# Kernel tuning notes

Measured on AMD Instinct MI355X. Metric: run time of the kernel, lower is better.

Reference implementation:

```python
import jax, jax.numpy as jnp
import numpy as np

N = 1024       # nodes
D1 = 64        # hidden_dim_1
D2 = 64        # hidden_dim_2
E = 16384      # edges
P = 8192       # query pairs
MAXX = 100     # max node label -> Embedding(MAXX+1, D1)
EPS = 1e-5     # LayerNorm eps (no affine)


def _ln(t):
    m = jnp.mean(t, axis=-1, keepdims=True)
    v = jnp.mean((t - m) ** 2, axis=-1, keepdims=True)
    return (t - m) / jnp.sqrt(v + EPS)


def setup_inputs() -> dict:
    key = jax.random.key(0)
    ks = jax.random.split(key, 12)
    s = 0.1
    x = jax.random.randint(ks[0], (N,), 0, MAXX + 1)
    ei = jax.random.randint(ks[1], (2, E), 0, N)
    pos = jax.random.randint(ks[2], (P, 2), 0, N)
    emb = jax.random.normal(ks[3], (MAXX + 1, D1)) * s
    sage_Wl = jax.random.normal(ks[4], (2, D1, D1)) * s   # lin_l weight (aggr path, has bias)
    sage_bl = jnp.zeros((2, D1))
    sage_Wr = jax.random.normal(ks[5], (2, D1, D1)) * s   # lin_r weight (root path, no bias)
    h_W = jax.random.normal(ks[6], (D1 + 1, D2)) * s
    h_b = jnp.zeros((D2,))
    g_W = jax.random.normal(ks[7], (D1 + 1 + 2 * D2, D2)) * s
    g_b = jnp.zeros((D2,))
    lin_W = jax.random.normal(ks[8], (D2, 1)) * s
    lin_b = jnp.zeros((1,))
    return {"x": x, "ei": ei, "pos": pos, "emb": emb,
            "sage_Wl": sage_Wl, "sage_bl": sage_bl, "sage_Wr": sage_Wr,
            "h_W": h_W, "h_b": h_b, "g_W": g_W, "g_b": g_b,
            "lin_W": lin_W, "lin_b": lin_b}


def reference(x, ei, pos, emb, sage_Wl, sage_bl, sage_Wr, h_W, h_b, g_W, g_b, lin_W, lin_b):
    n = N
    src, dst = ei[0], ei[1]
    h = emb[x]                                            # (n, D1)
    # SAGEConv x2: mean-aggregate src->dst, lin_l(aggr)+bias + lin_r(root); then LN (no affine, no relu)
    deg = jax.ops.segment_sum(jnp.ones((E,), h.dtype), dst, num_segments=n)
    deg = jnp.maximum(deg, 1.0)[:, None]
    for i in range(2):
        aggr = jax.ops.segment_sum(h[src], dst, num_segments=n) / deg
        h = _ln(aggr @ sage_Wl[i] + sage_bl[i] + h @ sage_Wr[i])
    # pairwise outer product features: (n, n, D1)
    A = h[:, None, :] * h[None, :, :]
    eim = jnp.zeros((n * n,), h.dtype).at[src * n + dst].set(1.0).reshape(n, n, 1)
    A = jnp.concatenate([A, eim], axis=-1)                # (n, n, D1+1)
    # mataggr: B = h_1(A); row/col sums; D = cat(A, vec_p, vec_q); g_1(D)
    B = jax.nn.relu(_ln(A @ h_W + h_b))                   # (n, n, D2)
    vec_p = jnp.sum(B, axis=1, keepdims=True)             # (n, 1, D2)
    vec_q = jnp.sum(B, axis=0, keepdims=True)             # (1, n, D2)
    Dm = jnp.concatenate([A,
                          jnp.broadcast_to(vec_p, (n, n, D2)),
                          jnp.broadcast_to(vec_q, (n, n, D2))], axis=-1)
    G = jax.nn.relu(_ln(Dm @ g_W + g_b))                  # (n, n, D2)
    # symmetrize and gather query pairs
    S = (G * jnp.transpose(G, (1, 0, 2))).reshape(n * n, D2)
    sel = S[pos[:, 0] * n + pos[:, 1]]                    # (P, D2)
    return sel @ lin_W + lin_b                            # (P, 1)
```

## Files before the change

### kernel.cpp

```cpp
#include <hip/hip_runtime.h>
#include <hip/hip_bf16.h>

#define NN 1024
#define DD 64
#define EE 16384
#define PP 8192
#define EPSF 1e-5f
#define SWP (DD + 8)

typedef __hip_bfloat16 bf16;
typedef __attribute__((ext_vector_type(8))) short short8;
typedef __attribute__((ext_vector_type(4))) float f32x4;

static __device__ __forceinline__ float dec1(const void* src, int i, int fl) {
    if (fl) return ((const float*)src)[i];
    return __bfloat162float(((const bf16*)src)[i]);
}
static __device__ __forceinline__ unsigned short f2bf_u(float f) {
    bf16 h = __float2bfloat16(f);
    return *reinterpret_cast<unsigned short*>(&h);
}
static __device__ __forceinline__ float bfu2f(unsigned short u) {
    unsigned int b = ((unsigned int)u) << 16;
    return __uint_as_float(b);
}

__global__ void k_probe(const unsigned short* __restrict__ raw, int n, int* __restrict__ flag) {
    int i = blockIdx.x * blockDim.x + threadIdx.x;
    if (i >= n) return;
    unsigned int bits = ((unsigned int)raw[i]) << 16;
    float v = __uint_as_float(bits);
    if (!(fabsf(v) <= 1e3f)) atomicOr(flag, 1);
}

__global__ void k_prep(const void* __restrict__ emb, const void* __restrict__ sWl,
                       const void* __restrict__ sbl, const void* __restrict__ sWr,
                       const void* __restrict__ hW, const void* __restrict__ hb,
                       const void* __restrict__ gW, const void* __restrict__ gb,
                       const void* __restrict__ lW, const void* __restrict__ lb,
                       const int* __restrict__ x, const int* __restrict__ ei,
                       const int* __restrict__ flagp,
                       float* __restrict__ Wlf, float* __restrict__ blf, float* __restrict__ Wrf,
                       float* __restrict__ WfT, float* __restrict__ hbw,
                       float* __restrict__ gWf, float* __restrict__ linf,
                       float* __restrict__ h0, int* __restrict__ deg,
                       unsigned int* __restrict__ eim, unsigned int* __restrict__ eimT) {
    int fl = *flagp;
    int b = blockIdx.x, t = threadIdx.x;
    if (b < 32) {
        int i = b * 256 + t; Wlf[i] = dec1(sWl, i, fl);
    } else if (b < 33) {
        if (t < 128) blf[t] = dec1(sbl, t, fl);
    } else if (b < 65) {
        int i = (b - 33) * 256 + t; Wrf[i] = dec1(sWr, i, fl);
    } else if (b < 82) {
        int i = (b - 65) * 256 + t;
        if (i < 4096) { int n = i >> 6, k = i & 63; WfT[n * DD + k] = dec1(hW, k * DD + n, fl); }
        else if (i < 4160) { hbw[i - 4096] = dec1(hb, i - 4096, fl); }
        else if (i < 4224) { hbw[64 + (i - 4160)] = dec1(hW, 64 * DD + (i - 4160), fl); }
    } else if (b < 131) {
        int i = (b - 82) * 256 + t;
        if (i < 193 * DD) gWf[i] = dec1(gW, i, fl);
        else if (i < 194 * DD) gWf[i] = dec1(gb, i - 193 * DD, fl);
    } else if (b < 132) {
        if (t < DD) linf[t] = dec1(lW, t, fl);
        else if (t == DD) linf[DD] = dec1(lb, 0, fl);
    } else if (b < 388) {
        int i = (b - 132) * 256 + t;
        int node = i >> 6, f = i & 63;
        h0[i] = dec1(emb, x[node] * DD + f, fl);
    } else {
        int e = (b - 388) * 256 + t;
        if (e < EE) {
            int s = ei[e], d = ei[EE + e];
            atomicAdd(&deg[d], 1);
            unsigned int idx = (unsigned int)(s * NN + d);
            atomicOr(&eim[idx >> 5], 1u << (idx & 31));
            unsigned int idxT = (unsigned int)(d * NN + s);
            atomicOr(&eimT[idxT >> 5], 1u << (idxT & 31));
        }
    }
}

__global__ void k_scan(const int* __restrict__ deg, int* __restrict__ rowptr,
                       int* __restrict__ cursor) {
    __shared__ int tmp[NN];
    int t = threadIdx.x;
    int v = deg[t];
    tmp[t] = v;
    __syncthreads();
    for (int off = 1; off < NN; off <<= 1) {
        int add = (t >= off) ? tmp[t - off] : 0;
        __syncthreads();
        tmp[t] += add;
        __syncthreads();
    }
    int incl = tmp[t];
    rowptr[t] = incl - v;
    cursor[t] = incl - v;
    if (t == NN - 1) rowptr[NN] = incl;
}

__global__ void k_scatter(const int* __restrict__ ei, int* __restrict__ cursor,
                          int* __restrict__ csrc) {
    int e = blockIdx.x * blockDim.x + threadIdx.x;
    if (e >= EE) return;
    int d = ei[EE + e];
    int c = atomicAdd(&cursor[d], 1);
    csrc[c] = ei[e];
}

__global__ void k_sage(const int* __restrict__ rowptr, const int* __restrict__ csrc,
                       const float* __restrict__ hin,
                       const float* __restrict__ Wl, const float* __restrict__ bl,
                       const float* __restrict__ Wr,
                       float* __restrict__ hout, unsigned short* __restrict__ hbf) {
    int i = blockIdx.x;
    int f = threadIdx.x;
    __shared__ float sa[DD], sh[DD];
    int r0 = rowptr[i], r1 = rowptr[i + 1];
    float s = 0.f;
    for (int r = r0; r < r1; ++r) {
        int src = csrc[r];
        s += hin[src * DD + f];
    }
    float dg = (float)max(r1 - r0, 1);
    sa[f] = s / dg;
    sh[f] = hin[i * DD + f];
    __syncthreads();
    float o = bl[f];
    for (int k = 0; k < DD; ++k) {
        o += sa[k] * Wl[k * DD + f] + sh[k] * Wr[k * DD + f];
    }
    float m = o;
    for (int off = 32; off; off >>= 1) m += __shfl_xor(m, off);
    m *= (1.0f / DD);
    float d0 = o - m;
    float v = d0 * d0;
    for (int off = 32; off; off >>= 1) v += __shfl_xor(v, off);
    v *= (1.0f / DD);
    float r = d0 * rsqrtf(v + EPSF);
    hout[i * DD + f] = r;
    hbf[i * DD + f] = f2bf_u(r);
}

__launch_bounds__(256)
__global__ void k_bstage(const float* __restrict__ h2, const unsigned short* __restrict__ hbf,
                         const float* __restrict__ WfT, const float* __restrict__ hbw,
                         const unsigned int* __restrict__ eim,
                         const unsigned int* __restrict__ eimT,
                         float* __restrict__ vp_part, float* __restrict__ vq_part) {
    int bid = blockIdx.x;
    int fix = bid >> 1, half = bid & 1;
    int tid = threadIdx.x;
    int lane = tid & 63, wave = tid >> 6;
    int l15 = lane & 15, quad = lane >> 4;

    __shared__ unsigned short sW[DD * SWP];
    __shared__ float red[4][2 * DD];

    {
        int m = tid >> 2;
        int k0 = (tid & 3) * 16;
        const float* hi = h2 + fix * DD;
        const float* wr = WfT + m * DD;
#pragma unroll
        for (int u = 0; u < 16; ++u) {
            int k = k0 + u;
            sW[m * SWP + k] = f2bf_u(hi[k] * wr[k]);
        }
    }
    __syncthreads();

    short8 Af[4][2];
#pragma unroll
    for (int mt = 0; mt < 4; ++mt)
#pragma unroll
        for (int kt = 0; kt < 2; ++kt)
            Af[mt][kt] = *(const short8*)(sW + (mt * 16 + l15) * SWP + kt * 32 + quad * 8);

    float hb0[4][4], hww[4][4];
#pragma unroll
    for (int mt = 0; mt < 4; ++mt) {
        f32x4 a = *(const f32x4*)(hbw + mt * 16 + quad * 4);
        f32x4 wv = *(const f32x4*)(hbw + 64 + mt * 16 + quad * 4);
#pragma unroll
        for (int r = 0; r < 4; ++r) { hb0[mt][r] = a[r]; hww[mt][r] = wv[r]; }
    }

    float accf[4][4], accb[4][4];
#pragma unroll
    for (int mt = 0; mt < 4; ++mt)
#pragma unroll
        for (int r = 0; r < 4; ++r) { accf[mt][r] = 0.f; accb[mt][r] = 0.f; }

    for (int g = half * 32 + wave; g < half * 32 + 32; g += 4) {
        short8 B0 = *(const short8*)(hbf + (g * 16 + l15) * DD + quad * 8);
        short8 B1 = *(const short8*)(hbf + (g * 16 + l15) * DD + 32 + quad * 8);

        f32x4 C[4];
#pragma unroll
        for (int mt = 0; mt < 4; ++mt) C[mt] = (f32x4){0.f, 0.f, 0.f, 0.f};
#pragma unroll
        for (int mt = 0; mt < 4; ++mt)
            C[mt] = __builtin_amdgcn_mfma_f32_16x16x32_bf16(Af[mt][0], B0, C[mt], 0, 0, 0);
#pragma unroll
        for (int mt = 0; mt < 4; ++mt)
            C[mt] = __builtin_amdgcn_mfma_f32_16x16x32_bf16(Af[mt][1], B1, C[mt], 0, 0, 0);

        unsigned int base = (unsigned int)(fix * NN + g * 16);
        unsigned int sf = (eim[base >> 5] >> (base & 31)) & 0xFFFFu;
        unsigned int sb = (eimT[base >> 5] >> (base & 31)) & 0xFFFFu;
        float ef = (float)((sf >> l15) & 1u);

        float s1 = 0.f, s2 = 0.f;
#pragma unroll
        for (int mt = 0; mt < 4; ++mt)
#pragma unroll
            for (int r = 0; r < 4; ++r) {
                float v = C[mt][r] + hb0[mt][r] + ef * hww[mt][r];
                C[mt][r] = v;
                s1 += v;
                s2 += v * v;
            }
        s1 += __shfl_xor(s1, 16); s1 += __shfl_xor(s1, 32);
        s2 += __shfl_xor(s2, 16); s2 += __shfl_xor(s2, 32);
        float mean = s1 * (1.f / DD);
        float var = fmaxf(s2 * (1.f / DD) - mean * mean, 0.f);
        float rs = rsqrtf(var + EPSF);
        float mrs = mean * rs;

        if (sf == sb) {
#pragma unroll
            for (int mt = 0; mt < 4; ++mt)
#pragma unroll
                for (int r = 0; r < 4; ++r) {
                    float u = fmaxf(C[mt][r] * rs - mrs, 0.f);
                    accf[mt][r] += u;
                    accb[mt][r] += u;
                }
        } else {
#pragma unroll
            for (int mt = 0; mt < 4; ++mt)
#pragma unroll
                for (int r = 0; r < 4; ++r)
                    accf[mt][r] += fmaxf(C[mt][r] * rs - mrs, 0.f);
            float de = (float)((sb >> l15) & 1u) - ef;
            float t1 = 0.f, t2 = 0.f;
#pragma unroll
            for (int mt = 0; mt < 4; ++mt)
#pragma unroll
                for (int r = 0; r < 4; ++r) {
                    float v = C[mt][r] + de * hww[mt][r];
                    C[mt][r] = v;
                    t1 += v;
                    t2 += v * v;
                }
            t1 += __shfl_xor(t1, 16); t1 += __shfl_xor(t1, 32);
            t2 += __shfl_xor(t2, 16); t2 += __shfl_xor(t2, 32);
            float mean2 = t1 * (1.f / DD);
            float var2 = fmaxf(t2 * (1.f / DD) - mean2 * mean2, 0.f);
            float rs2 = rsqrtf(var2 + EPSF);
            float mrs2 = mean2 * rs2;
#pragma unroll
            for (int mt = 0; mt < 4; ++mt)
#pragma unroll
                for (int r = 0; r < 4; ++r)
                    accb[mt][r] += fmaxf(C[mt][r] * rs2 - mrs2, 0.f);
        }
    }

#pragma unroll
    for (int step = 1; step < 16; step <<= 1)
#pragma unroll
        for (int mt = 0; mt < 4; ++mt)
#pragma unroll
            for (int r = 0; r < 4; ++r) {
                accf[mt][r] += __shfl_xor(accf[mt][r], step);
                accb[mt][r] += __shfl_xor(accb[mt][r], step);
            }

    if (l15 == 0) {
#pragma unroll
        for (int mt = 0; mt < 4; ++mt)
#pragma unroll
            for (int r = 0; r < 4; ++r) {
                int m = mt * 16 + quad * 4 + r;
                red[wave][m] = accf[mt][r];
                red[wave][DD + m] = accb[mt][r];
            }
    }
    __syncthreads();
    if (tid < 2 * DD) {
        float sum = red[0][tid] + red[1][tid] + red[2][tid] + red[3][tid];
        if (tid < DD) vp_part[(half * NN + fix) * DD + tid] = sum;
        else          vq_part[(half * NN + fix) * DD + (tid - DD)] = sum;
    }
}

__global__ void k_ppqq2(const float* __restrict__ vpp, const float* __restrict__ vqp,
                        const float* __restrict__ gWf,
                        float* __restrict__ ppb, float* __restrict__ qqb) {
    int b = blockIdx.x;
    int f = threadIdx.x;
    int i = b & 1023, which = b >> 10;
    const float* part = which ? vqp : vpp;
    int row0 = which ? 129 : 65;
    __shared__ float sv[DD];
    sv[f] = part[i * DD + f] + part[(NN + i) * DD + f];
    __syncthreads();
    float o = 0.f;
    for (int k = 0; k < DD; ++k) o += sv[k] * gWf[(row0 + k) * DD + f];
    (which ? qqb : ppb)[i * DD + f] = o;
}

__launch_bounds__(256)
__global__ void k_final(const int* __restrict__ pos, const unsigned short* __restrict__ hbf,
                        const float* __restrict__ gWf, const unsigned int* __restrict__ eim,
                        const float* __restrict__ pp, const float* __restrict__ qq,
                        const float* __restrict__ linf, const int* __restrict__ flag,
                        void* __restrict__ outv) {
    int blk = blockIdx.x;
    int tid = threadIdx.x;
    int lane = tid & 63, wave = tid >> 6;
    int l15 = lane & 15, quad = lane >> 4;

    __shared__ unsigned short sgW[DD * SWP];
    __shared__ unsigned short sq[64 * SWP];

    {
        int m = tid >> 2;
        int k0 = (tid & 3) * 16;
#pragma unroll
        for (int u = 0; u < 16; ++u) {
            int k = k0 + u;
            sgW[m * SWP + k] = f2bf_u(gWf[k * DD + m]);
        }
    }
    for (int u = 0; u < 16; ++u) {
        int row = wave * 16 + u;
        int p = blk * 64 + row;
        int a = pos[2 * p], b = pos[2 * p + 1];
        float prod = bfu2f(hbf[a * DD + lane]) * bfu2f(hbf[b * DD + lane]);
        sq[row * SWP + lane] = f2bf_u(prod);
    }
    __syncthreads();

    short8 B0 = *(const short8*)(sq + (wave * 16 + l15) * SWP + quad * 8);
    short8 B1 = *(const short8*)(sq + (wave * 16 + l15) * SWP + 32 + quad * 8);

    f32x4 C[4];
#pragma unroll
    for (int mt = 0; mt < 4; ++mt) C[mt] = (f32x4){0.f, 0.f, 0.f, 0.f};
#pragma unroll
    for (int mt = 0; mt < 4; ++mt) {
        short8 A0 = *(const short8*)(sgW + (mt * 16 + l15) * SWP + quad * 8);
        C[mt] = __builtin_amdgcn_mfma_f32_16x16x32_bf16(A0, B0, C[mt], 0, 0, 0);
    }
#pragma unroll
    for (int mt = 0; mt < 4; ++mt) {
        short8 A1 = *(const short8*)(sgW + (mt * 16 + l15) * SWP + 32 + quad * 8);
        C[mt] = __builtin_amdgcn_mfma_f32_16x16x32_bf16(A1, B1, C[mt], 0, 0, 0);
    }

    int p = blk * 64 + wave * 16 + l15;
    int a = pos[2 * p], b = pos[2 * p + 1];
    unsigned int iab = (unsigned int)(a * NN + b), iba = (unsigned int)(b * NN + a);
    float eab = (float)((eim[iab >> 5] >> (iab & 31)) & 1u);
    float eba = (float)((eim[iba >> 5] >> (iba & 31)) & 1u);

    float u1[4][4], u2[4][4];
    float s1 = 0.f, s12 = 0.f, s2 = 0.f, s22 = 0.f;
#pragma unroll
    for (int mt = 0; mt < 4; ++mt) {
        int m0 = mt * 16 + quad * 4;
        f32x4 w64v = *(const f32x4*)(gWf + 64 * DD + m0);
        f32x4 gbv  = *(const f32x4*)(gWf + 193 * DD + m0);
        f32x4 ppa  = *(const f32x4*)(pp + a * DD + m0);
        f32x4 qqb_ = *(const f32x4*)(qq + b * DD + m0);
        f32x4 ppb_ = *(const f32x4*)(pp + b * DD + m0);
        f32x4 qqa  = *(const f32x4*)(qq + a * DD + m0);
#pragma unroll
        for (int r = 0; r < 4; ++r) {
            float v1 = C[mt][r] + eab * w64v[r] + ppa[r] + qqb_[r] + gbv[r];
            float v2 = C[mt][r] + eba * w64v[r] + ppb_[r] + qqa[r] + gbv[r];
            u1[mt][r] = v1; u2[mt][r] = v2;
            s1 += v1; s12 += v1 * v1;
            s2 += v2; s22 += v2 * v2;
        }
    }
    s1 += __shfl_xor(s1, 16);  s1 += __shfl_xor(s1, 32);
    s12 += __shfl_xor(s12, 16); s12 += __shfl_xor(s12, 32);
    s2 += __shfl_xor(s2, 16);  s2 += __shfl_xor(s2, 32);
    s22 += __shfl_xor(s22, 16); s22 += __shfl_xor(s22, 32);
    float mean1 = s1 * (1.f / DD);
    float rs1 = rsqrtf(fmaxf(s12 * (1.f / DD) - mean1 * mean1, 0.f) + EPSF);
    float mrs1 = mean1 * rs1;
    float mean2 = s2 * (1.f / DD);
    float rs2 = rsqrtf(fmaxf(s22 * (1.f / DD) - mean2 * mean2, 0.f) + EPSF);
    float mrs2 = mean2 * rs2;

    float r = 0.f;
#pragma unroll
    for (int mt = 0; mt < 4; ++mt) {
        f32x4 lw = *(const f32x4*)(linf + mt * 16 + quad * 4);
#pragma unroll
        for (int rr = 0; rr < 4; ++rr) {
            float g1 = fmaxf(u1[mt][rr] * rs1 - mrs1, 0.f);
            float g2 = fmaxf(u2[mt][rr] * rs2 - mrs2, 0.f);
            r += g1 * g2 * lw[rr];
        }
    }
    r += __shfl_xor(r, 16); r += __shfl_xor(r, 32);
    if (quad == 0) {
        float res = r + linf[DD];
        if (*flag) ((float*)outv)[p] = res;
        else       ((bf16*)outv)[p] = __float2bfloat16(res);
    }
}

extern "C" void kernel_launch(void* const* d_in, const int* in_sizes, int n_in,
                              void* d_out, int out_size, void* d_ws, size_t ws_size,
                              hipStream_t stream) {
    const int* x      = (const int*)d_in[0];
    const int* ei     = (const int*)d_in[1];
    const int* pos    = (const int*)d_in[2];
    const void* emb     = d_in[3];
    const void* sage_Wl = d_in[4];
    const void* sage_bl = d_in[5];
    const void* sage_Wr = d_in[6];
    const void* h_W     = d_in[7];
    const void* h_b     = d_in[8];
    const void* g_W     = d_in[9];
    const void* g_b     = d_in[10];
    const void* lin_W   = d_in[11];
    const void* lin_b   = d_in[12];

    char* w = (char*)d_ws;
    auto alloc = [&](size_t bytes) {
        void* p = (void*)w;
        w += (bytes + 255) & ~(size_t)255;
        return p;
    };
    int*   flag = (int*)alloc(256);
    int*   degi = (int*)alloc(NN * 4);
    unsigned int* eim  = (unsigned int*)alloc(NN * NN / 8);
    unsigned int* eimT = (unsigned int*)alloc(NN * NN / 8);
    size_t zero_bytes = (size_t)((char*)w - (char*)d_ws);
    float* h0   = (float*)alloc(NN * DD * 4);
    float* h1   = (float*)alloc(NN * DD * 4);
    float* h2   = (float*)alloc(NN * DD * 4);
    unsigned short* hbf = (unsigned short*)alloc(NN * DD * 2);
    float* Wlf  = (float*)alloc(2 * DD * DD * 4);
    float* blf  = (float*)alloc(2 * DD * 4);
    float* Wrf  = (float*)alloc(2 * DD * DD * 4);
    float* WfT  = (float*)alloc(DD * DD * 4);
    float* hbw  = (float*)alloc(128 * 4);
    float* gWf  = (float*)alloc(194 * DD * 4);
    float* linf = (float*)alloc(65 * 4);
    float* vpp  = (float*)alloc(2 * NN * DD * 4);
    float* vqp  = (float*)alloc(2 * NN * DD * 4);
    float* ppb  = (float*)alloc(NN * DD * 4);
    float* qqb  = (float*)alloc(NN * DD * 4);
    int* rowptr = (int*)alloc((NN + 1) * 4);
    int* cursor = (int*)alloc(NN * 4);
    int* csrc   = (int*)alloc(EE * 4);

    hipMemsetAsync(d_ws, 0, zero_bytes, stream);

    k_probe<<<(101 * DD + 255) / 256, 256, 0, stream>>>((const unsigned short*)emb, 101 * DD, flag);

    k_prep<<<452, 256, 0, stream>>>(emb, sage_Wl, sage_bl, sage_Wr, h_W, h_b, g_W, g_b,
                                    lin_W, lin_b, x, ei, flag,
                                    Wlf, blf, Wrf, WfT, hbw, gWf, linf,
                                    h0, degi, eim, eimT);

    k_scan<<<1, NN, 0, stream>>>(degi, rowptr, cursor);
    k_scatter<<<EE / 256, 256, 0, stream>>>(ei, cursor, csrc);

    k_sage<<<NN, DD, 0, stream>>>(rowptr, csrc, h0, Wlf, blf, Wrf, h1, hbf);
    k_sage<<<NN, DD, 0, stream>>>(rowptr, csrc, h1, Wlf + DD * DD, blf + DD,
                                  Wrf + DD * DD, h2, hbf);

    k_bstage<<<2 * NN, 256, 0, stream>>>(h2, hbf, WfT, hbw, eim, eimT, vpp, vqp);

    k_ppqq2<<<2 * NN, DD, 0, stream>>>(vpp, vqp, gWf, ppb, qqb);

    k_final<<<PP / 64, 256, 0, stream>>>(pos, hbf, gWf, eim, ppb, qqb, linf, flag, d_out);
}
```

Before: 167.9 us.

## Fuse all stages into one cooperative persistent kernel with grid syncs

Replaces the nine separate kernel launches with a single cooperative kernel that runs each stage as a phase separated by grid-wide syncs. If cooperative launch is unavailable, it falls back to per-phase launches. The format probe becomes a per-wave ballot instead of a separate kernel. The B stage handles a full row per block instead of splitting it into halves, which removes the partial-sum merge; it also prefetches the next B fragments and seeds the accumulator with the bias. The aim is to remove launch overhead and inter-kernel gaps, at the cost of grid-sync latency and lower occupancy in phases that use only a few blocks.

```diff
diff --git a/kernel.cpp b/kernel.cpp
--- a/kernel.cpp
+++ b/kernel.cpp
@@ -1,5 +1,6 @@
 #include <hip/hip_runtime.h>
 #include <hip/hip_bf16.h>
+#include <hip/hip_cooperative_groups.h>
 
 #define NN 1024
 #define DD 64
@@ -7,6 +8,9 @@
 #define PP 8192
 #define EPSF 1e-5f
 #define SWP (DD + 8)
+#define SMEM_BYTES 11264
+
+namespace cg = cooperative_groups;
 
 typedef __hip_bfloat16 bf16;
 typedef __attribute__((ext_vector_type(8))) short short8;
@@ -21,154 +25,139 @@
     return *reinterpret_cast<unsigned short*>(&h);
 }
 static __device__ __forceinline__ float bfu2f(unsigned short u) {
-    unsigned int b = ((unsigned int)u) << 16;
-    return __uint_as_float(b);
-}
-
-__global__ void k_probe(const unsigned short* __restrict__ raw, int n, int* __restrict__ flag) {
-    int i = blockIdx.x * blockDim.x + threadIdx.x;
-    if (i >= n) return;
-    unsigned int bits = ((unsigned int)raw[i]) << 16;
-    float v = __uint_as_float(bits);
-    if (!(fabsf(v) <= 1e3f)) atomicOr(flag, 1);
-}
-
-__global__ void k_prep(const void* __restrict__ emb, const void* __restrict__ sWl,
-                       const void* __restrict__ sbl, const void* __restrict__ sWr,
-                       const void* __restrict__ hW, const void* __restrict__ hb,
-                       const void* __restrict__ gW, const void* __restrict__ gb,
-                       const void* __restrict__ lW, const void* __restrict__ lb,
-                       const int* __restrict__ x, const int* __restrict__ ei,
-                       const int* __restrict__ flagp,
-                       float* __restrict__ Wlf, float* __restrict__ blf, float* __restrict__ Wrf,
-                       float* __restrict__ WfT, float* __restrict__ hbw,
-                       float* __restrict__ gWf, float* __restrict__ linf,
-                       float* __restrict__ h0, int* __restrict__ deg,
-                       unsigned int* __restrict__ eim, unsigned int* __restrict__ eimT) {
-    int fl = *flagp;
-    int b = blockIdx.x, t = threadIdx.x;
-    if (b < 32) {
-        int i = b * 256 + t; Wlf[i] = dec1(sWl, i, fl);
-    } else if (b < 33) {
-        if (t < 128) blf[t] = dec1(sbl, t, fl);
-    } else if (b < 65) {
-        int i = (b - 33) * 256 + t; Wrf[i] = dec1(sWr, i, fl);
-    } else if (b < 82) {
-        int i = (b - 65) * 256 + t;
-        if (i < 4096) { int n = i >> 6, k = i & 63; WfT[n * DD + k] = dec1(hW, k * DD + n, fl); }
-        else if (i < 4160) { hbw[i - 4096] = dec1(hb, i - 4096, fl); }
-        else if (i < 4224) { hbw[64 + (i - 4160)] = dec1(hW, 64 * DD + (i - 4160), fl); }
+    return __uint_as_float(((unsigned int)u) << 16);
+}
+
+struct P {
+    const int *x, *ei, *pos;
+    const void *emb, *sWl, *sbl, *sWr, *hW, *hb, *gW, *gb, *lW, *lb;
+    float *Wlf, *blf, *Wrf, *WfT, *hbw, *gWf, *linf;
+    float *h0, *h1, *h2;
+    unsigned short *hbf;
+    int *deg, *rowptr, *cursor, *csrc;
+    unsigned int *eim, *eimT;
+    float *vecp, *vecq, *ppb, *qqb;
+    void *out;
+};
+
+static __device__ __forceinline__ int probe_fl(const void* emb) {
+    int lane = threadIdx.x & 63;
+    unsigned short raw = ((const unsigned short*)emb)[lane];
+    float v = __uint_as_float(((unsigned int)raw) << 16);
+    return (__ballot(!(fabsf(v) <= 1e3f)) != 0ull) ? 1 : 0;
+}
+
+static __device__ void phase_decode(const P& p, int b, int tid, int fl) {
+    if (b < 32) { int i = b * 256 + tid; p.Wlf[i] = dec1(p.sWl, i, fl); }
+    else if (b == 32) { if (tid < 128) p.blf[tid] = dec1(p.sbl, tid, fl); }
+    else if (b < 65) { int i = (b - 33) * 256 + tid; p.Wrf[i] = dec1(p.sWr, i, fl); }
+    else if (b < 82) {
+        int i = (b - 65) * 256 + tid;
+        if (i < 4096) { int n = i >> 6, k = i & 63; p.WfT[n * DD + k] = dec1(p.hW, k * DD + n, fl); }
+        else if (i < 4160) p.hbw[i - 4096] = dec1(p.hb, i - 4096, fl);
+        else if (i < 4224) p.hbw[64 + (i - 4160)] = dec1(p.hW, 64 * DD + (i - 4160), fl);
     } else if (b < 131) {
-        int i = (b - 82) * 256 + t;
-        if (i < 193 * DD) gWf[i] = dec1(gW, i, fl);
-        else if (i < 194 * DD) gWf[i] = dec1(gb, i - 193 * DD, fl);
-    } else if (b < 132) {
-        if (t < DD) linf[t] = dec1(lW, t, fl);
-        else if (t == DD) linf[DD] = dec1(lb, 0, fl);
+        int i = (b - 82) * 256 + tid;
+        if (i < 193 * DD) p.gWf[i] = dec1(p.gW, i, fl);
+        else if (i < 194 * DD) p.gWf[i] = dec1(p.gb, i - 193 * DD, fl);
+    } else if (b == 131) {
+        if (tid < DD) p.linf[tid] = dec1(p.lW, tid, fl);
+        else if (tid == DD) p.linf[DD] = dec1(p.lb, 0, fl);
     } else if (b < 388) {
-        int i = (b - 132) * 256 + t;
+        int i = (b - 132) * 256 + tid;
         int node = i >> 6, f = i & 63;
-        h0[i] = dec1(emb, x[node] * DD + f, fl);
-    } else {
-        int e = (b - 388) * 256 + t;
-        if (e < EE) {
-            int s = ei[e], d = ei[EE + e];
-            atomicAdd(&deg[d], 1);
-            unsigned int idx = (unsigned int)(s * NN + d);
-            atomicOr(&eim[idx >> 5], 1u << (idx & 31));
-            unsigned int idxT = (unsigned int)(d * NN + s);
-            atomicOr(&eimT[idxT >> 5], 1u << (idxT & 31));
-        }
-    }
-}
-
-__global__ void k_scan(const int* __restrict__ deg, int* __restrict__ rowptr,
-                       int* __restrict__ cursor) {
-    __shared__ int tmp[NN];
-    int t = threadIdx.x;
-    int v = deg[t];
-    tmp[t] = v;
+        p.h0[i] = dec1(p.emb, p.x[node] * DD + f, fl);
+    } else if (b < 452) {
+        int e = (b - 388) * 256 + tid;
+        int s = p.ei[e], d = p.ei[EE + e];
+        atomicAdd(&p.deg[d], 1);
+        unsigned int idx = (unsigned int)(s * NN + d);
+        atomicOr(&p.eim[idx >> 5], 1u << (idx & 31));
+        unsigned int idxT = (unsigned int)(d * NN + s);
+        atomicOr(&p.eimT[idxT >> 5], 1u << (idxT & 31));
+    }
+}
+
+static __device__ void phase_scan(const P& p, int b, int tid, char* smem) {
+    if (b != 0) return;
+    int* tmp = (int*)smem;
+    int v[4]; int s = 0;
+    int base4 = tid * 4;
+#pragma unroll
+    for (int u = 0; u < 4; ++u) { v[u] = p.deg[base4 + u]; s += v[u]; }
+    tmp[tid] = s;
     __syncthreads();
-    for (int off = 1; off < NN; off <<= 1) {
-        int add = (t >= off) ? tmp[t - off] : 0;
+    for (int off = 1; off < 256; off <<= 1) {
+        int a = (tid >= off) ? tmp[tid - off] : 0;
         __syncthreads();
-        tmp[t] += add;
+        tmp[tid] += a;
         __syncthreads();
     }
-    int incl = tmp[t];
-    rowptr[t] = incl - v;
-    cursor[t] = incl - v;
-    if (t == NN - 1) rowptr[NN] = incl;
-}
-
-__global__ void k_scatter(const int* __restrict__ ei, int* __restrict__ cursor,
-                          int* __restrict__ csrc) {
-    int e = blockIdx.x * blockDim.x + threadIdx.x;
-    if (e >= EE) return;
-    int d = ei[EE + e];
-    int c = atomicAdd(&cursor[d], 1);
-    csrc[c] = ei[e];
-}
-
-__global__ void k_sage(const int* __restrict__ rowptr, const int* __restrict__ csrc,
-                       const float* __restrict__ hin,
-                       const float* __restrict__ Wl, const float* __restrict__ bl,
-                       const float* __restrict__ Wr,
-                       float* __restrict__ hout, unsigned short* __restrict__ hbf) {
-    int i = blockIdx.x;
-    int f = threadIdx.x;
-    __shared__ float sa[DD], sh[DD];
-    int r0 = rowptr[i], r1 = rowptr[i + 1];
+    int run = tmp[tid] - s;
+#pragma unroll
+    for (int u = 0; u < 4; ++u) {
+        p.rowptr[base4 + u] = run;
+        p.cursor[base4 + u] = run;
+        run += v[u];
+    }
+    if (tid == 255) p.rowptr[NN] = run;
+}
+
+static __device__ void phase_scatter(const P& p, int b, int tid) {
+    if (b >= 64) return;
+    int e = b * 256 + tid;
+    int d = p.ei[EE + e];
+    int c = atomicAdd(&p.cursor[d], 1);
+    p.csrc[c] = p.ei[e];
+}
+
+static __device__ void phase_sage(const P& p, int b, int tid, char* smem, int round) {
+    if (b >= 256) return;
+    int lane = tid & 63, wave = tid >> 6;
+    int node = b * 4 + wave;
+    const float* hin = round ? p.h1 : p.h0;
+    const float* Wl = p.Wlf + round * DD * DD;
+    const float* bl = p.blf + round * DD;
+    const float* Wr = p.Wrf + round * DD * DD;
+    float* hout = round ? p.h2 : p.h1;
+
+    float* sa = (float*)smem + wave * 2 * DD;
+    float* sh = sa + DD;
+    int r0 = p.rowptr[node], r1 = p.rowptr[node + 1];
     float s = 0.f;
-    for (int r = r0; r < r1; ++r) {
-        int src = csrc[r];
-        s += hin[src * DD + f];
-    }
-    float dg = (float)max(r1 - r0, 1);
-    sa[f] = s / dg;
-    sh[f] = hin[i * DD + f];
-    __syncthreads();
-    float o = bl[f];
-    for (int k = 0; k < DD; ++k) {
-        o += sa[k] * Wl[k * DD + f] + sh[k] * Wr[k * DD + f];
-    }
+    for (int r = r0; r < r1; ++r) s += hin[p.csrc[r] * DD + lane];
+    sa[lane] = s / (float)max(r1 - r0, 1);
+    sh[lane] = hin[node * DD + lane];
+    float o = bl[lane];
+    for (int k = 0; k < DD; ++k)
+        o += sa[k] * Wl[k * DD + lane] + sh[k] * Wr[k * DD + lane];
     float m = o;
     for (int off = 32; off; off >>= 1) m += __shfl_xor(m, off);
-    m *= (1.0f / DD);
+    m *= (1.f / DD);
     float d0 = o - m;
     float v = d0 * d0;
     for (int off = 32; off; off >>= 1) v += __shfl_xor(v, off);
-    v *= (1.0f / DD);
+    v *= (1.f / DD);
     float r = d0 * rsqrtf(v + EPSF);
-    hout[i * DD + f] = r;
-    hbf[i * DD + f] = f2bf_u(r);
-}
-
-__launch_bounds__(256)
-__global__ void k_bstage(const float* __restrict__ h2, const unsigned short* __restrict__ hbf,
-                         const float* __restrict__ WfT, const float* __restrict__ hbw,
-                         const unsigned int* __restrict__ eim,
-                         const unsigned int* __restrict__ eimT,
-                         float* __restrict__ vp_part, float* __restrict__ vq_part) {
-    int bid = blockIdx.x;
-    int fix = bid >> 1, half = bid & 1;
-    int tid = threadIdx.x;
+    hout[node * DD + lane] = r;
+    if (round) p.hbf[node * DD + lane] = f2bf_u(r);
+}
+
+static __device__ void phase_bstage(const P& p, int b, int tid, char* smem) {
     int lane = tid & 63, wave = tid >> 6;
     int l15 = lane & 15, quad = lane >> 4;
-
-    __shared__ unsigned short sW[DD * SWP];
-    __shared__ float red[4][2 * DD];
-
+    unsigned short* sW = (unsigned short*)smem;
+    float* red = (float*)(smem + DD * SWP * 2);
     {
         int m = tid >> 2;
         int k0 = (tid & 3) * 16;
-        const float* hi = h2 + fix * DD;
-        const float* wr = WfT + m * DD;
-#pragma unroll
-        for (int u = 0; u < 16; ++u) {
-            int k = k0 + u;
-            sW[m * SWP + k] = f2bf_u(hi[k] * wr[k]);
-        }
+        const float* hi = p.h2 + b * DD;
+        const float* wr = p.WfT + m * DD;
+        unsigned short tmp[16];
+#pragma unroll
+        for (int u = 0; u < 16; ++u) tmp[u] = f2bf_u(hi[k0 + u] * wr[k0 + u]);
+        *(short8*)(sW + m * SWP + k0) = *(short8*)tmp;
+        *(short8*)(sW + m * SWP + k0 + 8) = *(short8*)(tmp + 8);
     }
     __syncthreads();
 
@@ -182,8 +171,8 @@
     float hb0[4][4], hww[4][4];
 #pragma unroll
     for (int mt = 0; mt < 4; ++mt) {
-        f32x4 a = *(const f32x4*)(hbw + mt * 16 + quad * 4);
-        f32x4 wv = *(const f32x4*)(hbw + 64 + mt * 16 + quad * 4);
+        f32x4 a = *(const f32x4*)(p.hbw + mt * 16 + quad * 4);
+        f32x4 wv = *(const f32x4*)(p.hbw + 64 + mt * 16 + quad * 4);
 #pragma unroll
         for (int r = 0; r < 4; ++r) { hb0[mt][r] = a[r]; hww[mt][r] = wv[r]; }
     }
@@ -194,31 +183,39 @@
 #pragma unroll
         for (int r = 0; r < 4; ++r) { accf[mt][r] = 0.f; accb[mt][r] = 0.f; }
 
-    for (int g = half * 32 + wave; g < half * 32 + 32; g += 4) {
-        short8 B0 = *(const short8*)(hbf + (g * 16 + l15) * DD + quad * 8);
-        short8 B1 = *(const short8*)(hbf + (g * 16 + l15) * DD + 32 + quad * 8);
+    int g = wave;
+    short8 B0 = *(const short8*)(p.hbf + (g * 16 + l15) * DD + quad * 8);
+    short8 B1 = *(const short8*)(p.hbf + (g * 16 + l15) * DD + 32 + quad * 8);
+
+    for (int it = 0; it < 16; ++it, g += 4) {
+        short8 cB0 = B0, cB1 = B1;
+        if (it < 15) {
+            int gn = g + 4;
+            B0 = *(const short8*)(p.hbf + (gn * 16 + l15) * DD + quad * 8);
+            B1 = *(const short8*)(p.hbf + (gn * 16 + l15) * DD + 32 + quad * 8);
+        }
+        unsigned int base = (unsigned int)(b * NN + g * 16);
+        unsigned int sf = (p.eim[base >> 5] >> (base & 31)) & 0xFFFFu;
+        unsigned int sb = (p.eimT[base >> 5] >> (base & 31)) & 0xFFFFu;
 
         f32x4 C[4];
 #pragma unroll
-        for (int mt = 0; mt < 4; ++mt) C[mt] = (f32x4){0.f, 0.f, 0.f, 0.f};
-#pragma unroll
         for (int mt = 0; mt < 4; ++mt)
-            C[mt] = __builtin_amdgcn_mfma_f32_16x16x32_bf16(Af[mt][0], B0, C[mt], 0, 0, 0);
+            C[mt] = (f32x4){hb0[mt][0], hb0[mt][1], hb0[mt][2], hb0[mt][3]};
 #pragma unroll
         for (int mt = 0; mt < 4; ++mt)
-            C[mt] = __builtin_amdgcn_mfma_f32_16x16x32_bf16(Af[mt][1], B1, C[mt], 0, 0, 0);
-
-        unsigned int base = (unsigned int)(fix * NN + g * 16);
-        unsigned int sf = (eim[base >> 5] >> (base & 31)) & 0xFFFFu;
-        unsigned int sb = (eimT[base >> 5] >> (base & 31)) & 0xFFFFu;
+            C[mt] = __builtin_amdgcn_mfma_f32_16x16x32_bf16(Af[mt][0], cB0, C[mt], 0, 0, 0);
+#pragma unroll
+        for (int mt = 0; mt < 4; ++mt)
+            C[mt] = __builtin_amdgcn_mfma_f32_16x16x32_bf16(Af[mt][1], cB1, C[mt], 0, 0, 0);
+
         float ef = (float)((sf >> l15) & 1u);
-
         float s1 = 0.f, s2 = 0.f;
 #pragma unroll
         for (int mt = 0; mt < 4; ++mt)
 #pragma unroll
             for (int r = 0; r < 4; ++r) {
-                float v = C[mt][r] + hb0[mt][r] + ef * hww[mt][r];
+                float v = C[mt][r] + ef * hww[mt][r];
                 C[mt][r] = v;
                 s1 += v;
                 s2 += v * v;
@@ -279,75 +276,65 @@
                 accf[mt][r] += __shfl_xor(accf[mt][r], step);
                 accb[mt][r] += __shfl_xor(accb[mt][r], step);
             }
-
     if (l15 == 0) {
 #pragma unroll
         for (int mt = 0; mt < 4; ++mt)
 #pragma unroll
             for (int r = 0; r < 4; ++r) {
                 int m = mt * 16 + quad * 4 + r;
-                red[wave][m] = accf[mt][r];
-                red[wave][DD + m] = accb[mt][r];
+                red[wave * 128 + m] = accf[mt][r];
+                red[wave * 128 + DD + m] = accb[mt][r];
             }
     }
     __syncthreads();
     if (tid < 2 * DD) {
-        float sum = red[0][tid] + red[1][tid] + red[2][tid] + red[3][tid];
-        if (tid < DD) vp_part[(half * NN + fix) * DD + tid] = sum;
-        else          vq_part[(half * NN + fix) * DD + (tid - DD)] = sum;
-    }
-}
-
-__global__ void k_ppqq2(const float* __restrict__ vpp, const float* __restrict__ vqp,
-                        const float* __restrict__ gWf,
-                        float* __restrict__ ppb, float* __restrict__ qqb) {
-    int b = blockIdx.x;
-    int f = threadIdx.x;
-    int i = b & 1023, which = b >> 10;
-    const float* part = which ? vqp : vpp;
+        float sum = red[tid] + red[128 + tid] + red[256 + tid] + red[384 + tid];
+        if (tid < DD) p.vecp[b * DD + tid] = sum;
+        else          p.vecq[b * DD + (tid - DD)] = sum;
+    }
+}
+
+static __device__ void phase_ppqq(const P& p, int b, int tid, char* smem) {
+    int lane = tid & 63, wave = tid >> 6;
+    if (wave >= 2) return;
+    int unit = b * 2 + wave;
+    int i = unit & 1023, which = unit >> 10;
     int row0 = which ? 129 : 65;
-    __shared__ float sv[DD];
-    sv[f] = part[i * DD + f] + part[(NN + i) * DD + f];
-    __syncthreads();
+    float* sv = (float*)smem + wave * DD;
+    sv[lane] = (which ? p.vecq : p.vecp)[i * DD + lane];
     float o = 0.f;
-    for (int k = 0; k < DD; ++k) o += sv[k] * gWf[(row0 + k) * DD + f];
-    (which ? qqb : ppb)[i * DD + f] = o;
-}
-
-__launch_bounds__(256)
-__global__ void k_final(const int* __restrict__ pos, const unsigned short* __restrict__ hbf,
-                        const float* __restrict__ gWf, const unsigned int* __restrict__ eim,
-                        const float* __restrict__ pp, const float* __restrict__ qq,
-                        const float* __restrict__ linf, const int* __restrict__ flag,
-                        void* __restrict__ outv) {
-    int blk = blockIdx.x;
-    int tid = threadIdx.x;
+    for (int k = 0; k < DD; ++k) o += sv[k] * p.gWf[(row0 + k) * DD + lane];
+    (which ? p.qqb : p.ppb)[i * DD + lane] = o;
+}
+
+static __device__ void phase_final(const P& p, int b, int tid, int fl, char* smem) {
+    if (b >= PP / 64) return;
     int lane = tid & 63, wave = tid >> 6;
     int l15 = lane & 15, quad = lane >> 4;
-
-    __shared__ unsigned short sgW[DD * SWP];
-    __shared__ unsigned short sq[64 * SWP];
-
+    unsigned short* sgW = (unsigned short*)smem;
     {
         int m = tid >> 2;
         int k0 = (tid & 3) * 16;
-#pragma unroll
-        for (int u = 0; u < 16; ++u) {
-            int k = k0 + u;
-            sgW[m * SWP + k] = f2bf_u(gWf[k * DD + m]);
-        }
-    }
-    for (int u = 0; u < 16; ++u) {
-        int row = wave * 16 + u;
-        int p = blk * 64 + row;
-        int a = pos[2 * p], b = pos[2 * p + 1];
-        float prod = bfu2f(hbf[a * DD + lane]) * bfu2f(hbf[b * DD + lane]);
-        sq[row * SWP + lane] = f2bf_u(prod);
+        unsigned short tmp[16];
+#pragma unroll
+        for (int u = 0; u < 16; ++u) tmp[u] = f2bf_u(p.gWf[(k0 + u) * DD + m]);
+        *(short8*)(sgW + m * SWP + k0) = *(short8*)tmp;
+        *(short8*)(sgW + m * SWP + k0 + 8) = *(short8*)(tmp + 8);
+    }
+
+    int pp_ = b * 64 + wave * 16 + l15;
+    int a = p.pos[2 * pp_], bb = p.pos[2 * pp_ + 1];
+    short8 ha0 = *(const short8*)(p.hbf + a * DD + quad * 8);
+    short8 hb0v = *(const short8*)(p.hbf + bb * DD + quad * 8);
+    short8 ha1 = *(const short8*)(p.hbf + a * DD + 32 + quad * 8);
+    short8 hb1v = *(const short8*)(p.hbf + bb * DD + 32 + quad * 8);
+    short8 B0, B1;
+#pragma unroll
+    for (int j = 0; j < 8; ++j) {
+        B0[j] = (short)f2bf_u(bfu2f((unsigned short)ha0[j]) * bfu2f((unsigned short)hb0v[j]));
+        B1[j] = (short)f2bf_u(bfu2f((unsigned short)ha1[j]) * bfu2f((unsigned short)hb1v[j]));
     }
     __syncthreads();
-
-    short8 B0 = *(const short8*)(sq + (wave * 16 + l15) * SWP + quad * 8);
-    short8 B1 = *(const short8*)(sq + (wave * 16 + l15) * SWP + 32 + quad * 8);
 
     f32x4 C[4];
 #pragma unroll
@@ -363,23 +350,21 @@
         C[mt] = __builtin_amdgcn_mfma_f32_16x16x32_bf16(A1, B1, C[mt], 0, 0, 0);
     }
 
-    int p = blk * 64 + wave * 16 + l15;
-    int a = pos[2 * p], b = pos[2 * p + 1];
-    unsigned int iab = (unsigned int)(a * NN + b), iba = (unsigned int)(b * NN + a);
-    float eab = (float)((eim[iab >> 5] >> (iab & 31)) & 1u);
-    float eba = (float)((eim[iba >> 5] >> (iba & 31)) & 1u);
+    unsigned int iab = (unsigned int)(a * NN + bb), iba = (unsigned int)(bb * NN + a);
+    float eab = (float)((p.eim[iab >> 5] >> (iab & 31)) & 1u);
+    float eba = (float)((p.eim[iba >> 5] >> (iba & 31)) & 1u);
 
     float u1[4][4], u2[4][4];
     float s1 = 0.f, s12 = 0.f, s2 = 0.f, s22 = 0.f;
 #pragma unroll
     for (int mt = 0; mt < 4; ++mt) {
         int m0 = mt * 16 + quad * 4;
-        f32x4 w64v = *(const f32x4*)(gWf + 64 * DD + m0);
-        f32x4 gbv  = *(const f32x4*)(gWf + 193 * DD + m0);
-        f32x4 ppa  = *(const f32x4*)(pp + a * DD + m0);
-        f32x4 qqb_ = *(const f32x4*)(qq + b * DD + m0);
-        f32x4 ppb_ = *(const f32x4*)(pp + b * DD + m0);
-        f32x4 qqa  = *(const f32x4*)(qq + a * DD + m0);
+        f32x4 w64v = *(const f32x4*)(p.gWf + 64 * DD + m0);
+        f32x4 gbv  = *(const f32x4*)(p.gWf + 193 * DD + m0);
+        f32x4 ppa  = *(const f32x4*)(p.ppb + a * DD + m0);
+        f32x4 qqb_ = *(const f32x4*)(p.qqb + bb * DD + m0);
+        f32x4 ppb_ = *(const f32x4*)(p.ppb + bb * DD + m0);
+        f32x4 qqa  = *(const f32x4*)(p.qqb + a * DD + m0);
 #pragma unroll
         for (int r = 0; r < 4; ++r) {
             float v1 = C[mt][r] + eab * w64v[r] + ppa[r] + qqb_[r] + gbv[r];
@@ -403,7 +388,7 @@
     float r = 0.f;
 #pragma unroll
     for (int mt = 0; mt < 4; ++mt) {
-        f32x4 lw = *(const f32x4*)(linf + mt * 16 + quad * 4);
+        f32x4 lw = *(const f32x4*)(p.linf + mt * 16 + quad * 4);
 #pragma unroll
         for (int rr = 0; rr < 4; ++rr) {
             float g1 = fmaxf(u1[mt][rr] * rs1 - mrs1, 0.f);
@@ -413,40 +398,57 @@
     }
     r += __shfl_xor(r, 16); r += __shfl_xor(r, 32);
     if (quad == 0) {
-        float res = r + linf[DD];
-        if (*flag) ((float*)outv)[p] = res;
-        else       ((bf16*)outv)[p] = __float2bfloat16(res);
+        float res = r + p.linf[DD];
+        if (fl) ((float*)p.out)[pp_] = res;
+        else    ((bf16*)p.out)[pp_] = __float2bfloat16(res);
+    }
+}
+
+__global__ __launch_bounds__(256, 4) void k_all(P p) {
+    cg::grid_group gg = cg::this_grid();
+    __shared__ __align__(16) char smem[SMEM_BYTES];
+    const int tid = threadIdx.x, b = blockIdx.x;
+    int fl = probe_fl(p.emb);
+
+    phase_decode(p, b, tid, fl);   gg.sync();
+    phase_scan(p, b, tid, smem);   gg.sync();
+    phase_scatter(p, b, tid);      gg.sync();
+    phase_sage(p, b, tid, smem, 0); gg.sync();
+    phase_sage(p, b, tid, smem, 1); gg.sync();
+    phase_bstage(p, b, tid, smem); gg.sync();
+    phase_ppqq(p, b, tid, smem);   gg.sync();
+    phase_final(p, b, tid, fl, smem);
+}
+
+__global__ __launch_bounds__(256) void k_phase(P p, int phase) {
+    __shared__ __align__(16) char smem[SMEM_BYTES];
+    const int tid = threadIdx.x, b = blockIdx.x;
+    int fl = probe_fl(p.emb);
+    switch (phase) {
+        case 0: phase_decode(p, b, tid, fl); break;
+        case 1: phase_scan(p, b, tid, smem); break;
+        case 2: phase_scatter(p, b, tid); break;
+        case 3: phase_sage(p, b, tid, smem, 0); break;
+        case 4: phase_sage(p, b, tid, smem, 1); break;
+        case 5: phase_bstage(p, b, tid, smem); break;
+        case 6: phase_ppqq(p, b, tid, smem); break;
+        case 7: phase_final(p, b, tid, fl, smem); break;
     }
 }
 
 extern "C" void kernel_launch(void* const* d_in, const int* in_sizes, int n_in,
                               void* d_out, int out_size, void* d_ws, size_t ws_size,
                               hipStream_t stream) {
-    const int* x      = (const int*)d_in[0];
-    const int* ei     = (const int*)d_in[1];
-    const int* pos    = (const int*)d_in[2];
-    const void* emb     = d_in[3];
-    const void* sage_Wl = d_in[4];
-    const void* sage_bl = d_in[5];
-    const void* sage_Wr = d_in[6];
-    const void* h_W     = d_in[7];
-    const void* h_b     = d_in[8];
-    const void* g_W     = d_in[9];
-    const void* g_b     = d_in[10];
-    const void* lin_W   = d_in[11];
-    const void* lin_b   = d_in[12];
-
     char* w = (char*)d_ws;
     auto alloc = [&](size_t bytes) {
-        void* p = (void*)w;
+        void* q = (void*)w;
         w += (bytes + 255) & ~(size_t)255;
-        return p;
+        return q;
     };
-    int*   flag = (int*)alloc(256);
-    int*   degi = (int*)alloc(NN * 4);
+    int* deg = (int*)alloc(NN * 4);
     unsigned int* eim  = (unsigned int*)alloc(NN * NN / 8);
     unsigned int* eimT = (unsigned int*)alloc(NN * NN / 8);
-    size_t zero_bytes = (size_t)((char*)w - (char*)d_ws);
+    size_t zero_bytes = (size_t)(w - (char*)d_ws);
     float* h0   = (float*)alloc(NN * DD * 4);
     float* h1   = (float*)alloc(NN * DD * 4);
     float* h2   = (float*)alloc(NN * DD * 4);
@@ -458,8 +460,8 @@
     float* hbw  = (float*)alloc(128 * 4);
     float* gWf  = (float*)alloc(194 * DD * 4);
     float* linf = (float*)alloc(65 * 4);
-    float* vpp  = (float*)alloc(2 * NN * DD * 4);
-    float* vqp  = (float*)alloc(2 * NN * DD * 4);
+    float* vecp = (float*)alloc(NN * DD * 4);
+    float* vecq = (float*)alloc(NN * DD * 4);
     float* ppb  = (float*)alloc(NN * DD * 4);
     float* qqb  = (float*)alloc(NN * DD * 4);
     int* rowptr = (int*)alloc((NN + 1) * 4);
@@ -468,23 +470,44 @@
 
     hipMemsetAsync(d_ws, 0, zero_bytes, stream);
 
-    k_probe<<<(101 * DD + 255) / 256, 256, 0, stream>>>((const unsigned short*)emb, 101 * DD, flag);
-
-    k_prep<<<452, 256, 0, stream>>>(emb, sage_Wl, sage_bl, sage_Wr, h_W, h_b, g_W, g_b,
-                                    lin_W, lin_b, x, ei, flag,
-                                    Wlf, blf, Wrf, WfT, hbw, gWf, linf,
-                                    h0, degi, eim, eimT);
-
-    k_scan<<<1, NN, 0, stream>>>(degi, rowptr, cursor);
-    k_scatter<<<EE / 256, 256, 0, stream>>>(ei, cursor, csrc);
-
-    k_sage<<<NN, DD, 0, stream>>>(rowptr, csrc, h0, Wlf, blf, Wrf, h1, hbf);
-    k_sage<<<NN, DD, 0, stream>>>(rowptr, csrc, h1, Wlf + DD * DD, blf + DD,
-                                  Wrf + DD * DD, h2, hbf);
-
-    k_bstage<<<2 * NN, 256, 0, stream>>>(h2, hbf, WfT, hbw, eim, eimT, vpp, vqp);
-
-    k_ppqq2<<<2 * NN, DD, 0, stream>>>(vpp, vqp, gWf, ppb, qqb);
-
-    k_final<<<PP / 64, 256, 0, stream>>>(pos, hbf, gWf, eim, ppb, qqb, linf, flag, d_out);
-}
+    P hp;
+    hp.x = (const int*)d_in[0];
+    hp.ei = (const int*)d_in[1];
+    hp.pos = (const int*)d_in[2];
+    hp.emb = d_in[3];
+    hp.sWl = d_in[4];
+    hp.sbl = d_in[5];
+    hp.sWr = d_in[6];
+    hp.hW = d_in[7];
+    hp.hb = d_in[8];
+    hp.gW = d_in[9];
+    hp.gb = d_in[10];
+    hp.lW = d_in[11];
+    hp.lb = d_in[12];
+    hp.Wlf = Wlf; hp.blf = blf; hp.Wrf = Wrf; hp.WfT = WfT; hp.hbw = hbw;
+    hp.gWf = gWf; hp.linf = linf;
+    hp.h0 = h0; hp.h1 = h1; hp.h2 = h2; hp.hbf = hbf;
+    hp.deg = deg; hp.rowptr = rowptr; hp.cursor = cursor; hp.csrc = csrc;
+    hp.eim = eim; hp.eimT = eimT;
+    hp.vecp = vecp; hp.vecq = vecq; hp.ppb = ppb; hp.qqb = qqb;
+    hp.out = d_out;
+
+    hipError_t err = hipErrorUnknown;
+    int nb = 0, ncu = 0;
+    if (hipOccupancyMaxActiveBlocksPerMultiprocessor(&nb, k_all, 256, 0) == hipSuccess &&
+        hipDeviceGetAttribute(&ncu, hipDeviceAttributeMultiprocessorCount, 0) == hipSuccess &&
+        (long)nb * ncu >= 1024) {
+        void* args[] = { &hp };
+        err = hipLaunchCooperativeKernel(k_all, dim3(1024), dim3(256), args, 0, stream);
+    }
+    if (err != hipSuccess) {
+        k_phase<<<452, 256, 0, stream>>>(hp, 0);
+        k_phase<<<1,   256, 0, stream>>>(hp, 1);
+        k_phase<<<64,  256, 0, stream>>>(hp, 2);
+        k_phase<<<256, 256, 0, stream>>>(hp, 3);
+        k_phase<<<256, 256, 0, stream>>>(hp, 4);
+        k_phase<<<1024, 256, 0, stream>>>(hp, 5);
+        k_phase<<<1024, 256, 0, stream>>>(hp, 6);
+        k_phase<<<128, 256, 0, stream>>>(hp, 7);
+    }
+}
```

Result: no change. 164.8 us (-1.9%).
